# Performance work log

Hardware: AMD Instinct MI355X
Metric: run time of the kernel (lower is better)

Reference implementation:

```python
import jax, jax.numpy as jnp
import numpy as np

HID = 128      # hidden_features
NF = 32        # noise_features
NPL = NF // 4  # noise features per layer
RES = 512      # noise grid resolution
N = 262144     # number of query points


def leaky_relu(x):
    return jax.nn.leaky_relu(x, negative_slope=0.01)


def sample_bilinear(image, coords):
    """image: [M, H, W]; coords: [..., M, 2] -> [..., M]"""
    M, Hn, Wn = image.shape
    x = coords[..., 0] - 0.5
    y = coords[..., 1] - 0.5
    x0f = jnp.floor(x)
    y0f = jnp.floor(y)
    xw = x - x0f
    yw = y - y0f
    x0 = x0f.astype(jnp.int32) % Wn
    x1 = (x0f.astype(jnp.int32) + 1) % Wn
    y0 = y0f.astype(jnp.int32) % Hn
    y1 = (y0f.astype(jnp.int32) + 1) % Hn
    f = jnp.arange(M)  # broadcasts against [..., M] index arrays
    i00 = image[f, y0, x0]
    i01 = image[f, y0, x1]
    i10 = image[f, y1, x0]
    i11 = image[f, y1, x1]
    i0 = i00 + (i01 - i00) * xw
    i1 = i10 + (i11 - i10) * xw
    return i0 + (i1 - i0) * yw


def setup_inputs() -> dict:
    key = jax.random.key(0)
    ks = jax.random.split(key, 12)
    noise = jax.random.normal(ks[0], (NF, RES, RES), dtype=jnp.float32)
    coords = jax.random.normal(ks[1], (N, 2), dtype=jnp.float32)
    # NoiseTransforms param: randn * 0.05 * 2**i per feature
    scale = 0.05 * (2.0 ** np.arange(NF)).astype(np.float32)
    transformations = jax.random.normal(ks[2], (NF, 2, 2), dtype=jnp.float32) * scale[:, None, None]
    input_vec = jnp.ones((HID,), dtype=jnp.float32)
    s_lin = 1.0 / np.sqrt(HID)
    s_noise = 1.0 / np.sqrt(NPL)
    lw = jax.random.uniform(ks[3], (4, HID, HID), jnp.float32, -s_lin, s_lin)
    lb = jax.random.uniform(ks[4], (4, HID), jnp.float32, -s_lin, s_lin)
    lnw = jax.random.uniform(ks[5], (4, HID, NPL), jnp.float32, -s_noise, s_noise)
    tw1 = jax.random.uniform(ks[6], (HID, HID), jnp.float32, -s_lin, s_lin)
    tb1 = jax.random.uniform(ks[7], (HID,), jnp.float32, -s_lin, s_lin)
    tw2 = jax.random.uniform(ks[8], (1, HID), jnp.float32, -s_lin, s_lin)
    tb2 = jax.random.uniform(ks[9], (1,), jnp.float32, -s_lin, s_lin)
    return {"noise": noise, "coords": coords, "transformations": transformations,
            "input_vec": input_vec, "lw": lw, "lb": lb, "lnw": lnw,
            "tw1": tw1, "tb1": tb1, "tw2": tw2, "tb2": tb2}


def reference(noise, coords, transformations, input_vec, lw, lb, lnw, tw1, tb1, tw2, tb2):
    # noise coords: [..., NF, 2]
    noise_coords = jnp.einsum('...n,Mmn->...Mm', coords, transformations)
    noise_values = sample_bilinear(noise, noise_coords)  # [..., NF]
    x = input_vec  # [HID], broadcasts up through layer adds
    for i in range(4):
        nv = noise_values[..., i * NPL:(i + 1) * NPL]
        x = leaky_relu(jnp.einsum('...h,oh->...o', x, lw[i]) + lb[i]
                       + jnp.einsum('...n,on->...o', nv, lnw[i]))
    h = leaky_relu(jnp.einsum('...h,oh->...o', x, tw1) + tb1)
    return jnp.einsum('...h,oh->...o', h, tw2) + tb2  # [..., 1]
```

## Files before the change

### kernel.cpp

```cpp
#include <hip/hip_runtime.h>

typedef _Float16 f16;
typedef f16 f16x4 __attribute__((ext_vector_type(4)));
typedef f16 f16x8 __attribute__((ext_vector_type(8)));
typedef float f32x4 __attribute__((ext_vector_type(4)));

#define RES 512
#define PTS 128
#define XS  136
#define AS  16


__device__ __forceinline__
void pack_w_body(int g, const float* __restrict__ lw, const float* __restrict__ lnw,
                 const float* __restrict__ lb, const float* __restrict__ tw1,
                 const float* __restrict__ tb1, const float* __restrict__ ivec,
                 f16* __restrict__ wf, f16* __restrict__ waugf) {
    if (g < 10240) {
        const int L = g >> 11, r = g & 2047;
        const int lane = r & 63, frag = r >> 6;
        const int q = lane >> 4, l15 = lane & 15;
        const int mt = frag >> 2, c = frag & 3;
        const float* src = ((L < 4) ? (lw + L * 16384) : tw1)
                           + (mt * 16 + l15) * 128 + c * 32 + q * 8;
        f16x8 h;
        #pragma unroll
        for (int j = 0; j < 8; ++j) h[j] = (f16)src[j];
        *(f16x8*)(wf + (size_t)g * 8) = h;
    } else {
        const int ga = g - 10240;
        const int L = ga >> 9, r = ga & 511;
        const int lane = r & 63, mt = r >> 6;
        const int q = lane >> 4, l15 = lane & 15;
        const int row = mt * 16 + l15;
        f16x8 h = {};
        if (q == 0 && L < 4) {
            const float* src = lnw + L * 1024 + row * 8;
            #pragma unroll
            for (int j = 0; j < 8; ++j) h[j] = (f16)src[j];
        }
        if (q == 1) {
            if (L == 0) {
                float s = lb[row];
                const float4* w4 = (const float4*)(lw + row * 128);
                const float4* v4 = (const float4*)ivec;
                #pragma unroll 8
                for (int k = 0; k < 32; ++k) {
                    const float4 w = w4[k], v = v4[k];
                    s += w.x * v.x + w.y * v.y + w.z * v.z + w.w * v.w;
                }
                h[0] = (f16)s;
            } else {
                h[0] = (f16)((L < 4) ? lb[L * 128 + row] : tb1[row]);
            }
        }
        *(f16x8*)(waugf + (size_t)ga * 8) = h;
    }
}

__global__ __launch_bounds__(256)
void pack_all_k(const float* __restrict__ n, f16* __restrict__ q,
                const float* __restrict__ lw,  const float* __restrict__ lnw,
                const float* __restrict__ lb,  const float* __restrict__ tw1,
                const float* __restrict__ tb1, const float* __restrict__ ivec,
                f16* __restrict__ wf, f16* __restrict__ waugf) {
    const int b = blockIdx.x;
    if (b < 8192) {
        const int idx = b * 256 + threadIdx.x;
        const int qx = idx & 255, rest = idx >> 8;
        const int qy = rest & 255, m = rest >> 8;
        const float* src = n + ((size_t)m * 512 + 2 * qy) * 512 + 2 * qx;
        const float2 r0 = *(const float2*)(src);
        const float2 r1 = *(const float2*)(src + 512);
        f16x4 o; o[0]=(f16)r0.x; o[1]=(f16)r0.y; o[2]=(f16)r1.x; o[3]=(f16)r1.y;
        *(f16x4*)(q + (size_t)idx * 4) = o;
    } else {
        pack_w_body((b - 8192) * 256 + threadIdx.x, lw, lnw, lb, tw1, tb1, ivec, wf, waugf);
    }
}

__global__ __launch_bounds__(256)
void pack_w_k(const float* __restrict__ lw,  const float* __restrict__ lnw,
              const float* __restrict__ lb,  const float* __restrict__ tw1,
              const float* __restrict__ tb1, const float* __restrict__ ivec,
              f16* __restrict__ wf, f16* __restrict__ waugf) {
    pack_w_body(blockIdx.x * 256 + threadIdx.x, lw, lnw, lb, tw1, tb1, ivec, wf, waugf);
}

__device__ __forceinline__ float quad_tap(uint2 q, int sy, int sx) {
    unsigned w = sy ? q.y : q.x;
    w >>= (sx << 4);
    union { unsigned short u; f16 h; } cv; cv.u = (unsigned short)w;
    return (float)cv.h;
}

template <bool QUAD>
__global__ __launch_bounds__(256, 4)
void sample_kernel(const void* __restrict__ noise_v,
                   const float* __restrict__ coords,
                   const float* __restrict__ trans,
                   f16* __restrict__ nv_ws, const int Ntot)
{
    __shared__ float T_sh[128];
    const int t = threadIdx.x;
    if (t < 128) T_sh[t] = trans[t];
    __syncthreads();

    const int g = blockIdx.x & 7;
    const int pb = (blockIdx.x >> 3) * 1024 + t;

    int mk[4];
    if (g < 7) { mk[0] = g; mk[1] = g + 9; mk[2] = g + 17; mk[3] = g + 25; }
    else       { mk[0] = 7; mk[1] = 8;     mk[2] = 16;     mk[3] = 24;     }

    float2 c[4];
    #pragma unroll
    for (int j = 0; j < 4; ++j)
        c[j] = *(const float2*)(coords + (pb + 256 * j) * 2);

    float nvr[4][4];
    {
        #pragma clang fp contract(off)
        #pragma unroll
        for (int j = 0; j < 4; ++j) {
            const float cx = c[j].x;
            const float cy = c[j].y;
            #pragma unroll
            for (int k = 0; k < 4; ++k) {
                const int m = mk[k];
                const float T00 = T_sh[m*4+0], T01 = T_sh[m*4+1];
                const float T10 = T_sh[m*4+2], T11 = T_sh[m*4+3];
                const float p0x = T00 * cx;
                const float p0y = T10 * cx;
                const float ncx = __builtin_fmaf(T01, cy, p0x);
                const float ncy = __builtin_fmaf(T11, cy, p0y);
                const float u = ncx - 0.5f;
                const float v = ncy - 0.5f;
                const float xf = floorf(u), yf = floorf(v);
                const float xw = u - xf, yw = v - yf;
                int ix = (xf >= 2147483648.0f || xf < -2147483648.0f) ? (int)(-2147483647 - 1) : (int)xf;
                int iy = (yf >= 2147483648.0f || yf < -2147483648.0f) ? (int)(-2147483647 - 1) : (int)yf;
                const int x0 = ix & (RES - 1);
                const int x1 = (int)(((unsigned)ix + 1u) & (unsigned)(RES - 1));
                const int y0 = iy & (RES - 1);
                const int y1 = (int)(((unsigned)iy + 1u) & (unsigned)(RES - 1));
                float i00, i01, i10, i11;
                if constexpr (QUAD) {
                    const f16* pl = (const f16*)noise_v + (size_t)m * (256 * 256 * 4);
                    const int qx0 = x0 >> 1, sx0 = x0 & 1;
                    const int qx1 = x1 >> 1, sx1 = x1 & 1;
                    const int qy0 = y0 >> 1, sy0 = y0 & 1;
                    const int qy1 = y1 >> 1, sy1 = y1 & 1;
                    const uint2 qa = *(const uint2*)(pl + (qy0 * 256 + qx0) * 4);
                    const uint2 qb = *(const uint2*)(pl + (qy0 * 256 + qx1) * 4);
                    const uint2 qc = *(const uint2*)(pl + (qy1 * 256 + qx0) * 4);
                    const uint2 qd = *(const uint2*)(pl + (qy1 * 256 + qx1) * 4);
                    i00 = quad_tap(qa, sy0, sx0);
                    i01 = quad_tap(qb, sy0, sx1);
                    i10 = quad_tap(qc, sy1, sx0);
                    i11 = quad_tap(qd, sy1, sx1);
                } else {
                    const float* pl = (const float*)noise_v + (size_t)m * (RES * RES);
                    i00 = pl[y0 * RES + x0];
                    i01 = pl[y0 * RES + x1];
                    i10 = pl[y1 * RES + x0];
                    i11 = pl[y1 * RES + x1];
                }
                const float a0 = i00 + (i01 - i00) * xw;
                const float a1 = i10 + (i11 - i10) * xw;
                nvr[j][k] = a0 + (a1 - a0) * yw;
            }
        }
    }
    #pragma unroll
    for (int j = 0; j < 4; ++j) {
        #pragma unroll
        for (int k = 0; k < 4; ++k) {
            const int m = mk[k];
            const int slot = (m & 7) * 4 + (m >> 3);
            nv_ws[(size_t)slot * Ntot + pb + 256 * j] = (f16)nvr[j][k];
        }
    }
}

__global__ __launch_bounds__(256, 2)
void mlp_kernel(const f16* __restrict__ nv_ws,
                const f16* __restrict__ wf,
                const f16* __restrict__ waugf,
                const float* __restrict__ tw2,
                const float* __restrict__ tb2,
                float* __restrict__ out, const int Ntot)
{
    __shared__ f16 Wm[16384];
    __shared__ f16 Waug[4096];
    __shared__ f16 xa[PTS * XS];
    __shared__ f16 xaug[PTS * AS];
    __shared__ __align__(16) float tw2_sh[128];
    __shared__ float pp[2][PTS];

    const int t    = threadIdx.x;
    const int wave = t >> 6;
    const int lane = t & 63;
    const int q    = lane >> 4;
    const int l15  = lane & 15;
    const int wi   = wave >> 1;
    const int wj   = wave & 1;
    const int pbase = blockIdx.x * PTS;
    const int p = t >> 1, h = t & 1;

    if (t < 128) {
        tw2_sh[t] = tw2[t];
        xaug[t * AS + 8] = (f16)1.0f;
        #pragma unroll
        for (int c = 9; c < 16; ++c) xaug[t * AS + c] = (f16)0.0f;
    }
    const float tb2_0 = tb2[0];

    f16x8 nva, nvb;
    {
        const int P = pbase + p;
        #pragma unroll
        for (int j = 0; j < 8; ++j) {
            nva[j] = nv_ws[(size_t)(j * 4 + 2 * h)     * Ntot + P];
            nvb[j] = nv_ws[(size_t)(j * 4 + 2 * h + 1) * Ntot + P];
        }
    }
    if (h == 0) *(f16x8*)&xaug[p * AS] = nva;

    {
        const f16x8 a0 = *(const f16x8*)&waugf[t * 8];
        const f16x8 a1 = *(const f16x8*)&waugf[(t + 256) * 8];
        *(f16x8*)&Waug[t * 8]         = a0;
        *(f16x8*)&Waug[(t + 256) * 8] = a1;
    }
    __syncthreads();

    const f32x4 z4 = {0.f, 0.f, 0.f, 0.f};
    f32x4 acc[4][4];
    f16x8 wreg[8], areg[2];
    #pragma unroll 1
    for (int L = 0; L < 5; ++L) {
        if (L < 4) {
            const f16* wsrc = wf + (L + 1) * 16384;
            #pragma unroll
            for (int i = 0; i < 8; ++i)
                wreg[i] = *(const f16x8*)&wsrc[(t + i * 256) * 8];
            const f16* asrc = waugf + (L + 1) * 4096;
            areg[0] = *(const f16x8*)&asrc[t * 8];
            areg[1] = *(const f16x8*)&asrc[(t + 256) * 8];
        }

        if (L == 0) {
            #pragma unroll
            for (int pg = 0; pg < 4; ++pg)
                #pragma unroll
                for (int mtl = 0; mtl < 4; ++mtl) acc[pg][mtl] = z4;
        }
        if (L) {
            #pragma unroll
            for (int c = 0; c < 4; ++c) {
                const int kc = c * 32 + q * 8;
                f16x8 xb[4];
                #pragma unroll
                for (int pg = 0; pg < 4; ++pg)
                    xb[pg] = *(const f16x8*)&xa[(wi * 64 + pg * 16 + l15) * XS + kc];
                #pragma unroll
                for (int mtl = 0; mtl < 4; ++mtl) {
                    const f16x8 aw = *(const f16x8*)
                        &Wm[(((wj * 4 + mtl) * 4 + c) * 64 + lane) * 8];
                    #pragma unroll
                    for (int pg = 0; pg < 4; ++pg) {
                        const f32x4 ci = (c == 0) ? z4 : acc[pg][mtl];
                        acc[pg][mtl] = __builtin_amdgcn_mfma_f32_16x16x32_f16(aw, xb[pg], ci, 0, 0, 0);
                    }
                }
            }
        }
        {
            f16x8 xb[4] = {};
            if (q < 2) {
                #pragma unroll
                for (int pg = 0; pg < 4; ++pg)
                    xb[pg] = *(const f16x8*)&xaug[(wi * 64 + pg * 16 + l15) * AS + q * 8];
            }
            #pragma unroll
            for (int mtl = 0; mtl < 4; ++mtl) {
                const f16x8 aw = *(const f16x8*)&Waug[((wj * 4 + mtl) * 64 + lane) * 8];
                #pragma unroll
                for (int pg = 0; pg < 4; ++pg)
                    acc[pg][mtl] = __builtin_amdgcn_mfma_f32_16x16x32_f16(aw, xb[pg], acc[pg][mtl], 0, 0, 0);
            }
        }

        if (L < 4) {
            #pragma unroll
            for (int pg = 0; pg < 4; ++pg) {
                const int pr = (wi * 64 + pg * 16 + l15) * XS;
                #pragma unroll
                for (int mtl = 0; mtl < 4; ++mtl) {
                    f16x4 hv;
                    #pragma unroll
                    for (int r = 0; r < 4; ++r) {
                        float v = acc[pg][mtl][r];
                        v = fmaxf(v, 0.01f * v);
                        hv[r] = (f16)v;
                    }
                    *(f16x4*)&xa[pr + wj * 64 + mtl * 16 + q * 4] = hv;
                }
            }
            if (L < 3) {
                const int Ln = L + 1;
                if ((Ln >> 1) == h)
                    *(f16x8*)&xaug[p * AS] = (Ln & 1) ? nvb : nva;
            }
            __syncthreads();
            {
                #pragma unroll
                for (int i = 0; i < 8; ++i)
                    *(f16x8*)&Wm[(t + i * 256) * 8] = wreg[i];
                *(f16x8*)&Waug[t * 8]         = areg[0];
                *(f16x8*)&Waug[(t + 256) * 8] = areg[1];
            }
            __syncthreads();
        } else {
            #pragma unroll
            for (int pg = 0; pg < 4; ++pg) {
                float s = 0.f;
                #pragma unroll
                for (int mtl = 0; mtl < 4; ++mtl) {
                    const f32x4 w4 = *(const f32x4*)&tw2_sh[wj * 64 + mtl * 16 + q * 4];
                    #pragma unroll
                    for (int r = 0; r < 4; ++r) {
                        float v = acc[pg][mtl][r];
                        v = fmaxf(v, 0.01f * v);
                        s += w4[r] * v;
                    }
                }
                s += __shfl_xor(s, 16);
                s += __shfl_xor(s, 32);
                if (q == 0) pp[wj][wi * 64 + pg * 16 + l15] = s;
            }
            __syncthreads();
            if (t < 128)
                out[pbase + t] = pp[0][t] + pp[1][t] + tb2_0;
        }
    }
}

extern "C" void kernel_launch(void* const* d_in, const int* in_sizes, int n_in,
                              void* d_out, int out_size, void* d_ws, size_t ws_size,
                              hipStream_t stream) {
    const float* noise  = (const float*)d_in[0];
    const float* coords = (const float*)d_in[1];
    const float* trans  = (const float*)d_in[2];
    const float* ivec   = (const float*)d_in[3];
    const float* lw     = (const float*)d_in[4];
    const float* lb     = (const float*)d_in[5];
    const float* lnw    = (const float*)d_in[6];
    const float* tw1    = (const float*)d_in[7];
    const float* tb1    = (const float*)d_in[8];
    const float* tw2    = (const float*)d_in[9];
    const float* tb2    = (const float*)d_in[10];
    float* o            = (float*)d_out;

    const int N = in_sizes[1] / 2;
    f16* nv    = (f16*)d_ws;
    const size_t NV = (size_t)N * 32;
    f16* wfp   = nv + NV;
    f16* waugp = wfp + 5 * 16384;
    f16* qn    = waugp + 5 * 4096;
    const size_t need_full = (NV + 5 * 16384 + 5 * 4096
                              + (size_t)32 * 256 * 256 * 4) * sizeof(f16);

    if (ws_size >= need_full) {
        pack_all_k<<<8192 + 50, 256, 0, stream>>>(noise, qn, lw, lnw, lb, tw1, tb1,
                                                  ivec, wfp, waugp);
        sample_kernel<true><<<(N / 1024) * 8, 256, 0, stream>>>(qn, coords, trans, nv, N);
    } else {
        pack_w_k<<<50, 256, 0, stream>>>(lw, lnw, lb, tw1, tb1, ivec, wfp, waugp);
        sample_kernel<false><<<(N / 1024) * 8, 256, 0, stream>>>(noise, coords, trans, nv, N);
    }
    mlp_kernel<<<N / PTS, 256, 0, stream>>>(nv, wfp, waugp, tw2, tb2, o, N);
}
```

Baseline: 205.7 us.

## Keep MLP weight fragments in registers loaded from global instead of LDS staging

The MLP kernel no longer stages each layer's weight and augmentation matrices through shared memory. Each wave now loads its own MFMA weight fragments straight from global memory into registers, and prefetches the next layer's fragments right after the current layer's MFMAs. This removes the shared-memory write/read round trip for weights and frees about 40KB of LDS per block. In exchange, every wave issues redundant global loads that must hit in L2, the kernel uses many more VGPRs, and the launch bound that asked for at least 2 blocks per CU is dropped, which can lower occupancy. The noise kernel also gains a dead, unused temporary that has no effect.

```diff
diff --git a/kernel.cpp b/kernel.cpp
--- a/kernel.cpp
+++ b/kernel.cpp
@@ -167,8 +167,10 @@
                     i11 = pl[y1 * RES + x1];
                 }
                 const float a0 = i00 + (i01 - i00) * xw;
-                const float a1 = i10 + (i11 - i10) * xw;
-                nvr[j][k] = a0 + (a1 - a0) * yw;
+                const float a1 = i10 + (i10 - i10) * xw;
+                (void)a1;
+                const float a1r = i10 + (i11 - i10) * xw;
+                nvr[j][k] = a0 + (a1r - a0) * yw;
             }
         }
     }
@@ -183,7 +185,7 @@
     }
 }
 
-__global__ __launch_bounds__(256, 2)
+__global__ __launch_bounds__(256)
 void mlp_kernel(const f16* __restrict__ nv_ws,
                 const f16* __restrict__ wf,
                 const f16* __restrict__ waugf,
@@ -191,8 +193,6 @@
                 const float* __restrict__ tb2,
                 float* __restrict__ out, const int Ntot)
 {
-    __shared__ f16 Wm[16384];
-    __shared__ f16 Waug[4096];
     __shared__ f16 xa[PTS * XS];
     __shared__ f16 xaug[PTS * AS];
     __shared__ __align__(16) float tw2_sh[128];
@@ -227,29 +227,22 @@
     }
     if (h == 0) *(f16x8*)&xaug[p * AS] = nva;
 
-    {
-        const f16x8 a0 = *(const f16x8*)&waugf[t * 8];
-        const f16x8 a1 = *(const f16x8*)&waugf[(t + 256) * 8];
-        *(f16x8*)&Waug[t * 8]         = a0;
-        *(f16x8*)&Waug[(t + 256) * 8] = a1;
+    f16x8 wm[16], wa[4];
+    #pragma unroll
+    for (int mtl = 0; mtl < 4; ++mtl)
+        wa[mtl] = *(const f16x8*)&waugf[(size_t)((wj * 4 + mtl) * 64 + lane) * 8];
+    #pragma unroll
+    for (int i = 0; i < 16; ++i) {
+        const int mtl = i >> 2, c = i & 3;
+        wm[i] = *(const f16x8*)
+            &wf[(size_t)((32 + (wj * 4 + mtl) * 4 + c) * 64 + lane) * 8];
     }
     __syncthreads();
 
     const f32x4 z4 = {0.f, 0.f, 0.f, 0.f};
     f32x4 acc[4][4];
-    f16x8 wreg[8], areg[2];
     #pragma unroll 1
     for (int L = 0; L < 5; ++L) {
-        if (L < 4) {
-            const f16* wsrc = wf + (L + 1) * 16384;
-            #pragma unroll
-            for (int i = 0; i < 8; ++i)
-                wreg[i] = *(const f16x8*)&wsrc[(t + i * 256) * 8];
-            const f16* asrc = waugf + (L + 1) * 4096;
-            areg[0] = *(const f16x8*)&asrc[t * 8];
-            areg[1] = *(const f16x8*)&asrc[(t + 256) * 8];
-        }
-
         if (L == 0) {
             #pragma unroll
             for (int pg = 0; pg < 4; ++pg)
@@ -266,13 +259,20 @@
                     xb[pg] = *(const f16x8*)&xa[(wi * 64 + pg * 16 + l15) * XS + kc];
                 #pragma unroll
                 for (int mtl = 0; mtl < 4; ++mtl) {
-                    const f16x8 aw = *(const f16x8*)
-                        &Wm[(((wj * 4 + mtl) * 4 + c) * 64 + lane) * 8];
                     #pragma unroll
                     for (int pg = 0; pg < 4; ++pg) {
                         const f32x4 ci = (c == 0) ? z4 : acc[pg][mtl];
-                        acc[pg][mtl] = __builtin_amdgcn_mfma_f32_16x16x32_f16(aw, xb[pg], ci, 0, 0, 0);
+                        acc[pg][mtl] = __builtin_amdgcn_mfma_f32_16x16x32_f16(
+                            wm[mtl * 4 + c], xb[pg], ci, 0, 0, 0);
                     }
+                }
+            }
+            if (L < 4) {
+                #pragma unroll
+                for (int i = 0; i < 16; ++i) {
+                    const int mtl = i >> 2, c = i & 3;
+                    wm[i] = *(const f16x8*)
+                        &wf[(size_t)(((L + 1) * 32 + (wj * 4 + mtl) * 4 + c) * 64 + lane) * 8];
                 }
             }
         }
@@ -284,15 +284,21 @@
                     xb[pg] = *(const f16x8*)&xaug[(wi * 64 + pg * 16 + l15) * AS + q * 8];
             }
             #pragma unroll
-            for (int mtl = 0; mtl < 4; ++mtl) {
-                const f16x8 aw = *(const f16x8*)&Waug[((wj * 4 + mtl) * 64 + lane) * 8];
+            for (int mtl = 0; mtl < 4; ++mtl)
                 #pragma unroll
                 for (int pg = 0; pg < 4; ++pg)
-                    acc[pg][mtl] = __builtin_amdgcn_mfma_f32_16x16x32_f16(aw, xb[pg], acc[pg][mtl], 0, 0, 0);
+                    acc[pg][mtl] = __builtin_amdgcn_mfma_f32_16x16x32_f16(
+                        wa[mtl], xb[pg], acc[pg][mtl], 0, 0, 0);
+            if (L < 4) {
+                #pragma unroll
+                for (int mtl = 0; mtl < 4; ++mtl)
+                    wa[mtl] = *(const f16x8*)
+                        &waugf[(size_t)(((L + 1) * 8 + wj * 4 + mtl) * 64 + lane) * 8];
             }
         }
 
         if (L < 4) {
+            __syncthreads();
             #pragma unroll
             for (int pg = 0; pg < 4; ++pg) {
                 const int pr = (wi * 64 + pg * 16 + l15) * XS;
@@ -312,14 +318,6 @@
                 const int Ln = L + 1;
                 if ((Ln >> 1) == h)
                     *(f16x8*)&xaug[p * AS] = (Ln & 1) ? nvb : nva;
-            }
-            __syncthreads();
-            {
-                #pragma unroll
-                for (int i = 0; i < 8; ++i)
-                    *(f16x8*)&Wm[(t + i * 256) * 8] = wreg[i];
-                *(f16x8*)&Waug[t * 8]         = areg[0];
-                *(f16x8*)&Waug[(t + 256) * 8] = areg[1];
             }
             __syncthreads();
         } else {
```

After: 237.2 us. +15.3%, slower.
